# Performance work log

Measured on AMD Instinct MI355X. Metric: run time of the kernel, lower is better.

Reference implementation:

```python
import math
import jax, jax.numpy as jnp
import numpy as np

CANTOR_DEPTH = 8
CANTOR_TEMPERATURE = 1.0
SEQ_LEN = 4096


def _cantor_positions(depth_max):
    positions = [np.array([0.0, 1.0])]
    for _ in range(1, depth_max):
        prev = positions[-1]
        new = []
        for i in range(len(prev) - 1):
            left = prev[i]
            right = prev[i + 1]
            third = (right - left) / 3.0
            new.append(left)
            new.append(left + third)
        new.append(prev[-1])
        positions.append(np.array(new))
    return positions


def _cantor_indices(seq_len, depth_max):
    # indices[d] = unique sorted long indices of Cantor positions at depth d
    pos = _cantor_positions(depth_max)
    out = []
    for d in range(depth_max):
        idx = np.unique((pos[d] * (seq_len - 1)).astype(np.int64))
        out.append(jnp.asarray(idx))
    return out


# number of depths actually used in the forward loop
_N_DEPTHS = min(CANTOR_DEPTH, int(math.log2(SEQ_LEN)) + 2)
# get_cantor_indices caps depth at cantor_depth - 1 implicitly via list length
CANTOR_IDX = _cantor_indices(SEQ_LEN, CANTOR_DEPTH)


def setup_inputs() -> dict:
    key0 = jax.random.key(0)
    ks = jax.random.split(key0, 4)
    B, S, D = 8, SEQ_LEN, 512
    return {
        "query": jax.random.normal(ks[0], (B, S, D), dtype=jnp.float32),
        "key": jax.random.normal(ks[1], (B, S, D), dtype=jnp.float32),
        "value": jax.random.normal(ks[2], (B, S, D), dtype=jnp.float32),
        "t": jax.random.normal(ks[3], (B,), dtype=jnp.float32),
        "scale_weights": jnp.ones((CANTOR_DEPTH,), dtype=jnp.float32),
        "scale_temperature": jnp.ones((1,), dtype=jnp.float32),
    }


def reference(query, key, value, t, scale_weights, scale_temperature):
    D = key.shape[-1]
    inv_scale = 1.0 / (math.sqrt(D) * CANTOR_TEMPERATURE)
    scale_outputs = []
    for depth in range(_N_DEPTHS):
        idx = CANTOR_IDX[depth]            # static, <= 2^depth + 1 indices
        sk = key[:, idx]                   # [B, Nd, D] gather
        sv = value[:, idx]                 # [B, Nd, D]
        scores = jnp.einsum("bqd,bkd->bqk", query, sk) * inv_scale
        attn = jax.nn.softmax(scores, axis=-1)
        scale_outputs.append(jnp.einsum("bqk,bkd->bqd", attn, sv))
    stacked = jnp.stack(scale_outputs, axis=0)  # [depths, B, Q, D]
    w = jax.nn.softmax(scale_weights[: len(scale_outputs)] / scale_temperature[0])
    out = jnp.sum(stacked * w[:, None, None, None], axis=0)  # [B, Q, D]
    # torch .squeeze(1) is a no-op here since Q != 1
    return out
```

## Files before the change

kernel.cpp:

```cpp
#include <hip/hip_runtime.h>

#define NDEPTH 8
#define NK 129
#define SEQB 4096
#define DIM 512

typedef short bf16x8 __attribute__((ext_vector_type(8)));
typedef short bf16x4 __attribute__((ext_vector_type(4)));
typedef float f32x4  __attribute__((ext_vector_type(4)));

struct CTab {
    int uidx[NK]; int minD[NK];
    int sidx[NK];
    int SB[NDEPTH + 1];
    int count;
};

static constexpr CTab make_ctab() {
    CTab T{};
    double pos[NDEPTH][NK] = {}; int cnt[NDEPTH] = {};
    pos[0][0] = 0.0; pos[0][1] = 1.0; cnt[0] = 2;
    for (int d = 1; d < NDEPTH; ++d) {
        const int n = cnt[d - 1]; int m = 0;
        for (int i = 0; i < n - 1; ++i) {
            const double left = pos[d - 1][i], right = pos[d - 1][i + 1];
            const double third = (right - left) / 3.0;
            pos[d][m++] = left; pos[d][m++] = left + third;
        }
        pos[d][m++] = pos[d - 1][n - 1]; cnt[d] = m;
    }
    int idx[NDEPTH][NK] = {}; int icnt[NDEPTH] = {};
    for (int d = 0; d < NDEPTH; ++d) {
        int m = 0;
        for (int i = 0; i < cnt[d]; ++i) {
            const long long v = (long long)(pos[d][i] * 4095.0);
            bool dup = false;
            for (int k = 0; k < m; ++k) if (idx[d][k] == (int)v) dup = true;
            if (!dup) idx[d][m++] = (int)v;
        }
        icnt[d] = m;
    }
    int u[2 * NK] = {}; int un = 0;
    for (int d = 0; d < NDEPTH; ++d)
        for (int i = 0; i < icnt[d]; ++i) {
            const int v = idx[d][i]; bool f = false;
            for (int k = 0; k < un; ++k) if (u[k] == v) f = true;
            if (!f && un < 2 * NK) u[un++] = v;
        }
    for (int i = 1; i < un; ++i) {
        const int key = u[i]; int k = i - 1;
        while (k >= 0 && u[k] > key) { u[k + 1] = u[k]; --k; }
        u[k + 1] = key;
    }
    T.count = un;
    for (int i = 0; i < un && i < NK; ++i) {
        T.uidx[i] = u[i];
        int md = NDEPTH;
        for (int d = 0; d < NDEPTH && md == NDEPTH; ++d)
            for (int k = 0; k < icnt[d]; ++k)
                if (idx[d][k] == u[i]) { md = d; break; }
        T.minD[i] = md;
    }
    int n = 0;
    for (int d = 0; d < NDEPTH; ++d) {
        T.SB[d] = n;
        for (int i = 0; i < un && i < NK; ++i)
            if (T.minD[i] == d) T.sidx[n++] = T.uidx[i];
    }
    T.SB[NDEPTH] = n;
    return T;
}
static constexpr CTab h_ct = make_ctab();
static_assert(h_ct.count == NK, "cantor union size mismatch");
static_assert(h_ct.SB[NDEPTH] == NK, "sorted union size mismatch");
__device__ __constant__ CTab g_ct = h_ct;

__host__ __device__ constexpr int depth_of(int key) {
    int d = NDEPTH - 1;
    for (int x = NDEPTH - 1; x >= 0; --x) if (key < h_ct.SB[x + 1]) d = x;
    return d;
}

__device__ __forceinline__ short f2bf(float f) {
    union { float f; unsigned u; } v; v.f = f;
    unsigned r = v.u + 0x7fffu + ((v.u >> 16) & 1u);
    return (short)(r >> 16);
}

__device__ __forceinline__ void gl_lds16(const void* g, void* lds) {
    __builtin_amdgcn_global_load_lds(
        (const __attribute__((address_space(1))) unsigned int*)g,
        (__attribute__((address_space(3))) unsigned int*)lds, 16, 0, 0);
}

#define WSK_ELEMS (8 * 144 * 512)

__global__ __launch_bounds__(256) void ufa_prep(
    const float* __restrict__ K, const float* __restrict__ V,
    short* __restrict__ ws)
{
    short* wsK  = ws;
    short* wsVt = ws + WSK_ELEMS;
    if (blockIdx.x < 1152) {
        const int b = blockIdx.x / 144, key = blockIdx.x % 144;
        short* dst = wsK + ((size_t)b * 144 + key) * 512;
        if (key < NK) {
            const float* src = K + ((size_t)b * SEQB + g_ct.sidx[key]) * DIM;
            for (int i = threadIdx.x; i < 512; i += 256) dst[i] = f2bf(src[i]);
        } else {
            for (int i = threadIdx.x; i < 512; i += 256) dst[i] = 0;
        }
    } else {
        __shared__ float tr[16][132];
        const int id = blockIdx.x - 1152;
        const int b = id >> 5, dc = id & 31;
        const float* Vb = V + (size_t)b * SEQB * DIM + dc * 16;
        const int kk = (int)threadIdx.x >> 4, d = (int)threadIdx.x & 15;
        #pragma unroll
        for (int it = 0; it < 9; ++it) {
            const int k = it * 16 + kk;
            if (k < NK) tr[d][k] = Vb[(size_t)g_ct.sidx[k] * DIM + d];
        }
        __syncthreads();
        short* dst = wsVt + ((size_t)b * 512 + dc * 16) * 192;
        for (int idx = threadIdx.x; idx < 16 * 192; idx += 256) {
            const int dd = idx / 192, k = idx - dd * 192;
            dst[idx] = (k < NK) ? f2bf(tr[dd][k]) : (short)0;
        }
    }
}

#define KCH 18432
#define VCH 24576
#define CLDS_OFF 36864
#define CSTR 200
#define SMEM_BYTES 62976

__global__ __launch_bounds__(256, 2) void ufa_main(
    const float* __restrict__ Q, const short* __restrict__ ws,
    const float* __restrict__ SW, const float* __restrict__ ST,
    float* __restrict__ Out)
{
    __shared__ char smem[SMEM_BYTES];

    const short* wsK  = ws;
    const short* wsVt = ws + WSK_ELEMS;

    const int t    = (int)threadIdx.x;
    const int w    = t >> 6;
    const int lane = t & 63;
    const int m    = lane & 15;
    const int quad = lane >> 4;
    const int b    = (int)blockIdx.x >> 6;
    const int q0w  = (((int)blockIdx.x & 63) << 6) + w * 16;

    const short* wsKb  = wsK  + (size_t)b * 144 * 512;
    const short* wsVb  = wsVt + (size_t)b * 512 * 192;

    float wgt[NDEPTH];
    {
        const float it = 1.0f / ST[0];
        float mx = -3.0e38f;
        #pragma unroll
        for (int d = 0; d < NDEPTH; ++d) { wgt[d] = SW[d] * it; mx = fmaxf(mx, wgt[d]); }
        float sum = 0.0f;
        #pragma unroll
        for (int d = 0; d < NDEPTH; ++d) { wgt[d] = __expf(wgt[d] - mx); sum += wgt[d]; }
        const float is = 1.0f / sum;
        #pragma unroll
        for (int d = 0; d < NDEPTH; ++d) wgt[d] *= is;
    }

    #define STAGE_K(c, dst)                                                  \
        for (int g = w; g < 18; g += 4) {                                    \
            const int off  = g * 1024 + lane * 16;                           \
            const int row  = off >> 7;                                       \
            const int slot = (off >> 4) & 7;                                 \
            const int slog = slot ^ (row & 7);                               \
            gl_lds16(wsKb + (size_t)row * 512 + (c) * 64 + slog * 8,         \
                     (dst) + g * 1024);                                      \
        }
    #define STAGE_V(c2, dst)                                                 \
        for (int g = w; g < 24; g += 4) {                                    \
            const int off  = g * 1024 + lane * 16;                           \
            const int row  = off / 384;                                      \
            const int rem  = off - row * 384;                                \
            const int slot = rem >> 4;                                       \
            const int slog = (slot & ~7) | ((slot & 7) ^ (row & 7));         \
            gl_lds16(wsVb + (size_t)((c2) * 64 + row) * 192 + slog * 8,      \
                     (dst) + g * 1024);                                      \
        }

    char* const kbuf0 = smem;
    char* const kbuf1 = smem + KCH;

    STAGE_K(0, kbuf0);

    bf16x8 qf[16];
    const float* Qb = Q + ((size_t)b * SEQB + q0w + m) * DIM;
    #pragma unroll
    for (int ks = 0; ks < 16; ++ks) {
        const float* qp = Qb + ks * 32 + quad * 8;
        const float4 x = *(const float4*)qp;
        const float4 y = *(const float4*)(qp + 4);
        qf[ks][0] = f2bf(x.x); qf[ks][1] = f2bf(x.y);
        qf[ks][2] = f2bf(x.z); qf[ks][3] = f2bf(x.w);
        qf[ks][4] = f2bf(y.x); qf[ks][5] = f2bf(y.y);
        qf[ks][6] = f2bf(y.z); qf[ks][7] = f2bf(y.w);
    }
    __syncthreads();

    f32x4 acc[9];
    #pragma unroll
    for (int tt = 0; tt < 9; ++tt) acc[tt] = (f32x4){0.f, 0.f, 0.f, 0.f};

    for (int c = 0; c < 8; ++c) {
        if (c < 7) { STAGE_K(c + 1, (c & 1) ? kbuf0 : kbuf1); }
        const char* buf = (c & 1) ? kbuf1 : kbuf0;
        #pragma unroll
        for (int kk = 0; kk < 2; ++kk) {
            #pragma unroll
            for (int tt = 0; tt < 9; ++tt) {
                const int row  = tt * 16 + m;
                const int slog = (kk * 4 + quad) ^ (row & 7);
                const bf16x8 bk = *(const bf16x8*)(buf + row * 128 + slog * 16);
                acc[tt] = __builtin_amdgcn_mfma_f32_16x16x32_bf16(
                              bk, qf[c * 2 + kk], acc[tt], 0, 0, 0);
            }
        }
        __syncthreads();
    }

    STAGE_V(0, smem);

    const float inv_scale = 0.04419417382415922f;
    float ev[9][4];
    float mx = -3.0e38f;
    #pragma unroll
    for (int tt = 0; tt < 9; ++tt) {
        #pragma unroll
        for (int i = 0; i < 4; ++i) {
            float s = acc[tt][i] * inv_scale;
            if (tt == 8) s = (quad == 0 && i == 0) ? s : -3.0e38f;
            ev[tt][i] = s;
            mx = fmaxf(mx, s);
        }
    }
    mx = fmaxf(mx, __shfl_xor(mx, 16));
    mx = fmaxf(mx, __shfl_xor(mx, 32));

    float P[NDEPTH];
    #pragma unroll
    for (int d = 0; d < NDEPTH; ++d) P[d] = 0.0f;
    #pragma unroll
    for (int tt = 0; tt < 9; ++tt) {
        const int dLo = depth_of(tt * 16);
        const int dHi = depth_of(tt * 16 + 15 < NK ? tt * 16 + 15 : NK - 1);
        #pragma unroll
        for (int i = 0; i < 4; ++i) {
            const float e = __expf(ev[tt][i] - mx);
            ev[tt][i] = e;
            if (dLo == dHi) {
                P[dLo] += e;
            } else {
                const int key = tt * 16 + quad * 4 + i;
                #pragma unroll
                for (int d = dLo; d <= dHi; ++d) {
                    const bool in = (key >= h_ct.SB[d]) && (key < h_ct.SB[d + 1]);
                    P[d] += in ? e : 0.0f;
                }
            }
        }
    }
    #pragma unroll
    for (int d = 0; d < NDEPTH; ++d) {
        P[d] += __shfl_xor(P[d], 16);
        P[d] += __shfl_xor(P[d], 32);
    }

    float Lc = 0.0f, Tsf[NDEPTH];
    #pragma unroll
    for (int d = 0; d < NDEPTH; ++d) { Lc += P[d]; Tsf[d] = Lc; }
    {
        float ta = 0.0f;
        #pragma unroll
        for (int d = NDEPTH - 1; d >= 0; --d) { ta += wgt[d] / Tsf[d]; Tsf[d] = ta; }
    }

    short* crow = (short*)(smem + CLDS_OFF) + (w * 16 + m) * CSTR;
    #pragma unroll
    for (int tt = 0; tt < 9; ++tt) {
        const int dLo = depth_of(tt * 16);
        const int dHi = depth_of(tt * 16 + 15 < NK ? tt * 16 + 15 : NK - 1);
        bf16x4 pk;
        #pragma unroll
        for (int i = 0; i < 4; ++i) {
            float tv = Tsf[dLo];
            if (dLo != dHi) {
                const int key = tt * 16 + quad * 4 + i;
                #pragma unroll
                for (int d = dLo + 1; d <= dHi; ++d)
                    tv = (key >= h_ct.SB[d]) ? Tsf[d] : tv;
            }
            pk[i] = f2bf(ev[tt][i] * tv);
        }
        *(bf16x4*)(crow + tt * 16 + quad * 4) = pk;
    }
    *(bf16x4*)(crow + 144 + quad * 4) = (bf16x4){0, 0, 0, 0};

    __syncthreads();

    bf16x8 ac[5];
    {
        const short* cr = (const short*)(smem + CLDS_OFF) + (w * 16 + m) * CSTR;
        #pragma unroll
        for (int ks = 0; ks < 5; ++ks)
            ac[ks] = *(const bf16x8*)(cr + ks * 32 + quad * 8);
    }
    __syncthreads();

    char* const vbuf0 = smem;
    char* const vbuf1 = smem + VCH;
    float* Obm = Out + ((size_t)b * SEQB + q0w + m) * DIM + quad * 4;

    for (int c2 = 0; c2 < 8; ++c2) {
        if (c2 < 7) { STAGE_V(c2 + 1, (c2 & 1) ? vbuf0 : vbuf1); }
        const char* buf = (c2 & 1) ? vbuf1 : vbuf0;
        #pragma unroll
        for (int nt = 0; nt < 4; ++nt) {
            f32x4 o = (f32x4){0.f, 0.f, 0.f, 0.f};
            #pragma unroll
            for (int ks = 0; ks < 5; ++ks) {
                const int row  = nt * 16 + m;
                const int slot = ks * 4 + quad;
                const int slog = (slot & ~7) | ((slot & 7) ^ (row & 7));
                const bf16x8 bv = *(const bf16x8*)(buf + row * 384 + slog * 16);
                o = __builtin_amdgcn_mfma_f32_16x16x32_bf16(bv, ac[ks], o, 0, 0, 0);
            }
            *(f32x4*)(Obm + c2 * 64 + nt * 16) = o;
        }
        if (c2 < 7) __syncthreads();
    }
}

extern "C" void kernel_launch(void* const* d_in, const int* in_sizes, int n_in,
                              void* d_out, int out_size, void* d_ws, size_t ws_size,
                              hipStream_t stream) {
    const float* Q  = (const float*)d_in[0];
    const float* K  = (const float*)d_in[1];
    const float* V  = (const float*)d_in[2];
    const float* SW = (const float*)d_in[4];
    const float* ST = (const float*)d_in[5];
    float* Out = (float*)d_out;
    short* ws  = (short*)d_ws;

    ufa_prep<<<dim3(1152 + 256), dim3(256), 0, stream>>>(K, V, ws);
    ufa_main<<<dim3(512), dim3(256), 0, stream>>>(Q, ws, SW, ST, Out);
}
```

Measured before the change: 207.5 us.

## Triple-buffer K and V LDS staging with vmcnt-based waits and finer V chunks

Moves K and V staging in the main kernel from double to triple buffering with a prefetch distance of two. Full __syncthreads are replaced by explicit s_waitcnt vmcnt counts plus raw s_barrier, so the newest prefetch can stay in flight. V chunks are halved to 32 rows and the C matrix gets its own LDS region, which removes two barriers around the C round trip. The prep kernel now does vectorized float2 loads with packed bf16 stores. The hand-tuned vmcnt counts depend on exact load and store issue order and could be fragile.

```diff
diff --git a/kernel.cpp b/kernel.cpp
--- a/kernel.cpp
+++ b/kernel.cpp
@@ -93,6 +93,11 @@
         (__attribute__((address_space(3))) unsigned int*)lds, 16, 0, 0);
 }
 
+#define WAITVM(n) do {                                                   \
+        asm volatile("s_waitcnt vmcnt(" #n ")" ::: "memory");            \
+        __builtin_amdgcn_sched_barrier(0);                               \
+    } while (0)
+
 #define WSK_ELEMS (8 * 144 * 512)
 
 __global__ __launch_bounds__(256) void ufa_prep(
@@ -103,12 +108,14 @@
     short* wsVt = ws + WSK_ELEMS;
     if (blockIdx.x < 1152) {
         const int b = blockIdx.x / 144, key = blockIdx.x % 144;
-        short* dst = wsK + ((size_t)b * 144 + key) * 512;
+        unsigned* dst = (unsigned*)(wsK + ((size_t)b * 144 + key) * 512);
         if (key < NK) {
             const float* src = K + ((size_t)b * SEQB + g_ct.sidx[key]) * DIM;
-            for (int i = threadIdx.x; i < 512; i += 256) dst[i] = f2bf(src[i]);
+            const float2 s = *(const float2*)(src + threadIdx.x * 2);
+            dst[threadIdx.x] = ((unsigned)(unsigned short)f2bf(s.y) << 16)
+                             | (unsigned short)f2bf(s.x);
         } else {
-            for (int i = threadIdx.x; i < 512; i += 256) dst[i] = 0;
+            dst[threadIdx.x] = 0u;
         }
     } else {
         __shared__ float tr[16][132];
@@ -130,18 +137,18 @@
     }
 }
 
-#define KCH 18432
-#define VCH 24576
-#define CLDS_OFF 36864
+#define KCH 20480
+#define VCH 12288
+#define VB_BASE 25600
 #define CSTR 200
-#define SMEM_BYTES 62976
+#define SMEM_BYTES 62464
 
 __global__ __launch_bounds__(256, 2) void ufa_main(
     const float* __restrict__ Q, const short* __restrict__ ws,
     const float* __restrict__ SW, const float* __restrict__ ST,
     float* __restrict__ Out)
 {
-    __shared__ char smem[SMEM_BYTES];
+    __shared__ __align__(16) char smem[SMEM_BYTES];
 
     const short* wsK  = ws;
     const short* wsVt = ws + WSK_ELEMS;
@@ -154,8 +161,8 @@
     const int b    = (int)blockIdx.x >> 6;
     const int q0w  = (((int)blockIdx.x & 63) << 6) + w * 16;
 
-    const short* wsKb  = wsK  + (size_t)b * 144 * 512;
-    const short* wsVb  = wsVt + (size_t)b * 512 * 192;
+    const short* wsKb = wsK  + (size_t)b * 144 * 512;
+    const short* wsVb = wsVt + (size_t)b * 512 * 192;
 
     float wgt[NDEPTH];
     {
@@ -172,7 +179,7 @@
     }
 
     #define STAGE_K(c, dst)                                                  \
-        for (int g = w; g < 18; g += 4) {                                    \
+        for (int g = w; g < 20; g += 4) {                                    \
             const int off  = g * 1024 + lane * 16;                           \
             const int row  = off >> 7;                                       \
             const int slot = (off >> 4) & 7;                                 \
@@ -181,20 +188,18 @@
                      (dst) + g * 1024);                                      \
         }
     #define STAGE_V(c2, dst)                                                 \
-        for (int g = w; g < 24; g += 4) {                                    \
+        for (int g = w; g < 12; g += 4) {                                    \
             const int off  = g * 1024 + lane * 16;                           \
             const int row  = off / 384;                                      \
             const int rem  = off - row * 384;                                \
             const int slot = rem >> 4;                                       \
             const int slog = (slot & ~7) | ((slot & 7) ^ (row & 7));         \
-            gl_lds16(wsVb + (size_t)((c2) * 64 + row) * 192 + slog * 8,      \
+            gl_lds16(wsVb + (size_t)((c2) * 32 + row) * 192 + slog * 8,      \
                      (dst) + g * 1024);                                      \
         }
 
-    char* const kbuf0 = smem;
-    char* const kbuf1 = smem + KCH;
-
-    STAGE_K(0, kbuf0);
+    STAGE_K(0, smem);
+    STAGE_K(1, smem + KCH);
 
     bf16x8 qf[16];
     const float* Qb = Q + ((size_t)b * SEQB + q0w + m) * DIM;
@@ -215,8 +220,8 @@
     for (int tt = 0; tt < 9; ++tt) acc[tt] = (f32x4){0.f, 0.f, 0.f, 0.f};
 
     for (int c = 0; c < 8; ++c) {
-        if (c < 7) { STAGE_K(c + 1, (c & 1) ? kbuf0 : kbuf1); }
-        const char* buf = (c & 1) ? kbuf1 : kbuf0;
+        if (c < 6) { STAGE_K(c + 2, smem + ((c + 2) % 3) * KCH); }
+        const char* buf = smem + (c % 3) * KCH;
         #pragma unroll
         for (int kk = 0; kk < 2; ++kk) {
             #pragma unroll
@@ -228,10 +233,15 @@
                               bk, qf[c * 2 + kk], acc[tt], 0, 0, 0);
             }
         }
-        __syncthreads();
-    }
-
-    STAGE_V(0, smem);
+        if (c < 7) {
+            if (c < 6) { WAITVM(5); } else { WAITVM(0); }
+            __builtin_amdgcn_s_barrier();
+        }
+    }
+    __syncthreads();
+
+    STAGE_V(0, smem + VB_BASE);
+    STAGE_V(1, smem + VB_BASE + VCH);
 
     const float inv_scale = 0.04419417382415922f;
     float ev[9][4];
@@ -287,7 +297,7 @@
         for (int d = NDEPTH - 1; d >= 0; --d) { ta += wgt[d] / Tsf[d]; Tsf[d] = ta; }
     }
 
-    short* crow = (short*)(smem + CLDS_OFF) + (w * 16 + m) * CSTR;
+    short* crow = (short*)smem + (w * 16 + m) * CSTR;
     #pragma unroll
     for (int tt = 0; tt < 9; ++tt) {
         const int dLo = depth_of(tt * 16);
@@ -308,26 +318,22 @@
     }
     *(bf16x4*)(crow + 144 + quad * 4) = (bf16x4){0, 0, 0, 0};
 
-    __syncthreads();
-
     bf16x8 ac[5];
-    {
-        const short* cr = (const short*)(smem + CLDS_OFF) + (w * 16 + m) * CSTR;
-        #pragma unroll
-        for (int ks = 0; ks < 5; ++ks)
-            ac[ks] = *(const bf16x8*)(cr + ks * 32 + quad * 8);
-    }
-    __syncthreads();
-
-    char* const vbuf0 = smem;
-    char* const vbuf1 = smem + VCH;
+    #pragma unroll
+    for (int ks = 0; ks < 5; ++ks)
+        ac[ks] = *(const bf16x8*)(crow - m * CSTR + m * CSTR + ks * 32 + quad * 8);
+
+    asm volatile("s_waitcnt vmcnt(3) lgkmcnt(0)" ::: "memory");
+    __builtin_amdgcn_sched_barrier(0);
+    __builtin_amdgcn_s_barrier();
+
     float* Obm = Out + ((size_t)b * SEQB + q0w + m) * DIM + quad * 4;
 
-    for (int c2 = 0; c2 < 8; ++c2) {
-        if (c2 < 7) { STAGE_V(c2 + 1, (c2 & 1) ? vbuf0 : vbuf1); }
-        const char* buf = (c2 & 1) ? vbuf1 : vbuf0;
-        #pragma unroll
-        for (int nt = 0; nt < 4; ++nt) {
+    for (int c2 = 0; c2 < 16; ++c2) {
+        if (c2 < 14) { STAGE_V(c2 + 2, smem + VB_BASE + ((c2 + 2) % 3) * VCH); }
+        const char* buf = smem + VB_BASE + (c2 % 3) * VCH;
+        #pragma unroll
+        for (int nt = 0; nt < 2; ++nt) {
             f32x4 o = (f32x4){0.f, 0.f, 0.f, 0.f};
             #pragma unroll
             for (int ks = 0; ks < 5; ++ks) {
@@ -337,9 +343,12 @@
                 const bf16x8 bv = *(const bf16x8*)(buf + row * 384 + slog * 16);
                 o = __builtin_amdgcn_mfma_f32_16x16x32_bf16(bv, ac[ks], o, 0, 0, 0);
             }
-            *(f32x4*)(Obm + c2 * 64 + nt * 16) = o;
-        }
-        if (c2 < 7) __syncthreads();
+            *(f32x4*)(Obm + c2 * 32 + nt * 16) = o;
+        }
+        if (c2 < 15) {
+            if (c2 < 14) { WAITVM(5); } else { WAITVM(2); }
+            __builtin_amdgcn_s_barrier();
+        }
     }
 }
 
```

Result: no change. 206.4 us (-0.5%).
